# Optimization experiments

Measured on AMD Instinct MI355X. Metric: run time of the kernel, lower is better.

## Reference

```python
import jax, jax.numpy as jnp
import numpy as np


def _lstm(x, h0, c0, Wx, Wh, b):
    """Keras-order LSTM (gates i,f,c,o). x: [B,T,E] -> hidden seq [B,T,H]."""
    xw = jnp.einsum('bte,eg->btg', x, Wx) + b  # precompute input projections

    def step(carry, xw_t):
        h, c = carry
        z = xw_t + h @ Wh
        i, f, g, o = jnp.split(z, 4, axis=-1)
        c = jax.nn.sigmoid(f) * c + jax.nn.sigmoid(i) * jnp.tanh(g)
        h = jax.nn.sigmoid(o) * jnp.tanh(c)
        return (h, c), h

    _, hs = jax.lax.scan(step, (h0, c0), jnp.swapaxes(xw, 0, 1))
    return jnp.swapaxes(hs, 0, 1)


def setup_inputs() -> dict:
    key = jax.random.key(0)
    ks = jax.random.split(key, 16)
    V_IN = V_OUT = 32000
    E = 512      # embedding_dim
    H = 512      # encoder hidden_units per direction
    D = 2 * H    # decoder state width (matches BiLSTM output / attention dims)
    B, T_IN, T_OUT = 4, 128, 128
    s = 0.02

    def w(k, shape):
        return jax.random.normal(k, shape, jnp.float32) * s

    return {
        'input_seq': jax.random.randint(ks[0], (B, T_IN), 0, V_IN, jnp.int32),
        'output_seq': jax.random.randint(ks[1], (B, T_OUT), 0, V_OUT, jnp.int32),
        'enc_emb': w(ks[2], (V_IN, E)),
        'dec_emb': w(ks[3], (V_OUT, E)),
        'Wx_f': w(ks[4], (E, 4 * H)), 'Wh_f': w(ks[5], (H, 4 * H)), 'b_f': jnp.zeros((4 * H,), jnp.float32),
        'Wx_b': w(ks[6], (E, 4 * H)), 'Wh_b': w(ks[7], (H, 4 * H)), 'b_b': jnp.zeros((4 * H,), jnp.float32),
        'Wx_d': w(ks[8], (E, 4 * D)), 'Wh_d': w(ks[9], (D, 4 * D)), 'b_d': jnp.zeros((4 * D,), jnp.float32),
        'attn_scale': w(ks[10], (D,)),
        'Wo': w(ks[11], (D, V_OUT)), 'bo': jnp.zeros((V_OUT,), jnp.float32),
    }


def reference(input_seq, output_seq, enc_emb, dec_emb,
              Wx_f, Wh_f, b_f, Wx_b, Wh_b, b_b,
              Wx_d, Wh_d, b_d, attn_scale, Wo, bo):
    B = input_seq.shape[0]
    H = Wh_f.shape[0]
    D = 2 * H

    # --- encoder: BiLSTM, return_sequences=True ---
    enc_x = enc_emb[input_seq]                       # [B,Tin,E]
    z = jnp.zeros((B, H), jnp.float32)
    fwd = _lstm(enc_x, z, z, Wx_f, Wh_f, b_f)        # [B,Tin,H]
    bwd = _lstm(enc_x[:, ::-1], z, z, Wx_b, Wh_b, b_b)[:, ::-1]
    enc_out = jnp.concatenate([fwd, bwd], axis=-1)   # [B,Tin,2H]

    # --- decoder: LSTMCell-driven RNN, init state = last encoder output ---
    dec_x = dec_emb[output_seq]                      # [B,Tout,E]
    h0 = enc_out[:, -1, :]                           # [B,D]
    c0 = jnp.zeros((B, D), jnp.float32)
    dec_out = _lstm(dec_x, h0, c0, Wx_d, Wh_d, b_d)  # [B,Tout,D]

    # --- additive (Bahdanau) attention: query=dec_out, key=value=enc_out ---
    scores = jnp.einsum(
        'btsd,d->bts',
        jnp.tanh(dec_out[:, :, None, :] + enc_out[:, None, :, :]),
        attn_scale)                                  # [B,Tout,Tin]
    wts = jax.nn.softmax(scores, axis=-1)
    attn = jnp.einsum('bts,bsd->btd', wts, enc_out)  # [B,Tout,D]

    # --- output dense + softmax over vocab ---
    return jax.nn.softmax(attn @ Wo + bo, axis=-1)   # [B,Tout,V_out]
```

## Files before the change

### kernel.cpp

```cpp
#include <hip/hip_runtime.h>


typedef __attribute__((ext_vector_type(8))) short bf16x8;
typedef __attribute__((ext_vector_type(4))) float f32x4;

__device__ __forceinline__ short f2bf(float f) {
  unsigned u = __builtin_bit_cast(unsigned, f);
  u += 0x7fffu + ((u >> 16) & 1u);
  return (short)(u >> 16);
}
__device__ __forceinline__ float b2f(short s) {
  unsigned u = ((unsigned)(unsigned short)s) << 16;
  return __builtin_bit_cast(float, u);
}
__device__ __forceinline__ float sigf(float x) { return 1.f / (1.f + __expf(-x)); }
__device__ __forceinline__ float tanhf_fast(float x) {
  x = fminf(fmaxf(x, -15.f), 15.f);
  float e = __expf(2.f * x);
  return (e - 1.f) / (e + 1.f);
}

__device__ __forceinline__ unsigned ld_coh(const unsigned* p) {
  return __hip_atomic_load(p, __ATOMIC_RELAXED, __HIP_MEMORY_SCOPE_AGENT);
}
__device__ __forceinline__ void st_coh(unsigned* p, unsigned v) {
  __hip_atomic_store(p, v, __ATOMIC_RELAXED, __HIP_MEMORY_SCOPE_AGENT);
}

#define OFF_HBF   ((size_t)0)
#define OFF_HBB   (OFF_HBF + 2*2048*4)
#define OFF_HBD   (OFF_HBB + 2*2048*4)
#define OFF_ENCX  (OFF_HBD + 2*4096*4)
#define OFF_DECX  (OFF_ENCX + (size_t)64*512*8*2)
#define OFF_WXF   (OFF_DECX + (size_t)64*512*8*2)
#define OFF_WXB   (OFF_WXF + (size_t)512*2048*2)
#define OFF_WXD   (OFF_WXB + (size_t)512*2048*2)
#define OFF_WOS   (OFF_WXD + (size_t)512*4096*2)
#define OFF_XWF   (OFF_WOS + (size_t)1024*32000*2)
#define OFF_XWB   (OFF_XWF + (size_t)512*2048*4)
#define OFF_XWD   (OFF_XWB + (size_t)512*2048*4)
#define OFF_ENCO  (OFF_XWD + (size_t)512*4096*4)
#define OFF_ENCT  (OFF_ENCO + (size_t)4*128*1024*4)
#define OFF_DECO  (OFF_ENCT + (size_t)4*128*1024*4)
#define OFF_ATTN  (OFF_DECO + (size_t)4*128*1024*4)
#define OFF_LOG   (OFF_ATTN + (size_t)128*512*8*2)
#define WS_NEED   (OFF_LOG + (size_t)512*32000*2)

__device__ __forceinline__ void gather_body(const int* seq, const float* emb,
                                            short* dst, int bx, int by) {
  int m  = by * 64 + (threadIdx.x & 63);
  int e8 = bx * 4 + (threadIdx.x >> 6);
  int id = seq[m];
  const float* src = emb + (size_t)id * 512 + e8 * 8;
  bf16x8 v;
#pragma unroll
  for (int j = 0; j < 8; ++j) v[j] = f2bf(src[j]);
  *(bf16x8*)(dst + ((size_t)e8 * 512 + m) * 8) = v;
}

__device__ __forceinline__ void swz_body(const float* W, short* dst, int N,
                                         int k8, int n) {
  const float* src = W + (size_t)k8 * 8 * N + n;
  bf16x8 v;
#pragma unroll
  for (int j = 0; j < 8; ++j) v[j] = f2bf(src[(size_t)j * N]);
  *(bf16x8*)(dst + ((size_t)k8 * N + n) * 8) = v;
}

__device__ __forceinline__ void gemm_body(const short* __restrict__ A,
                                          const short* __restrict__ B,
                                          float* Cf, short* Cb,
                                          int M, int N, int K,
                                          int bx, int by, bool bf16out) {
  const int wv = threadIdx.x >> 6, lane = threadIdx.x & 63;
  const int q = lane >> 4, l15 = lane & 15;
  const int m0 = by * 128 + (wv >> 1) * 64;
  const int n0 = bx * 128 + (wv & 1) * 64;
  f32x4 acc[4][4];
#pragma unroll
  for (int i = 0; i < 4; ++i)
#pragma unroll
    for (int j = 0; j < 4; ++j) acc[i][j] = (f32x4){0.f, 0.f, 0.f, 0.f};
  const int KS = K >> 5;
  for (int ks = 0; ks < KS; ++ks) {
    const size_t k8 = (size_t)(ks * 4 + q);
    const short* Ap = A + (k8 * M + m0 + l15) * 8;
    const short* Bp = B + (k8 * N + n0 + l15) * 8;
    bf16x8 av[4], bv[4];
#pragma unroll
    for (int i = 0; i < 4; ++i) av[i] = *(const bf16x8*)(Ap + i * 128);
#pragma unroll
    for (int j = 0; j < 4; ++j) bv[j] = *(const bf16x8*)(Bp + j * 128);
#pragma unroll
    for (int i = 0; i < 4; ++i)
#pragma unroll
      for (int j = 0; j < 4; ++j)
        acc[i][j] = __builtin_amdgcn_mfma_f32_16x16x32_bf16(av[i], bv[j], acc[i][j], 0, 0, 0);
  }
#pragma unroll
  for (int i = 0; i < 4; ++i)
#pragma unroll
    for (int j = 0; j < 4; ++j)
#pragma unroll
      for (int r = 0; r < 4; ++r) {
        size_t idx = (size_t)(m0 + i * 16 + q * 4 + r) * N + (n0 + j * 16 + l15);
        if (bf16out) Cb[idx] = f2bf(acc[i][j][r]);
        else         Cf[idx] = acc[i][j][r];
      }
}

__global__ __launch_bounds__(256) void prep(
    const int* __restrict__ iseq, const int* __restrict__ oseq,
    const float* __restrict__ enc_emb, const float* __restrict__ dec_emb,
    const float* __restrict__ Wx_f, const float* __restrict__ Wx_b,
    const float* __restrict__ Wx_d,
    short* encx, short* decx, short* wxf_s, short* wxb_s, short* wxd_s) {
  int bid = blockIdx.x;
  if (bid < 128)        { gather_body(iseq, enc_emb, encx, bid & 15, bid >> 4); return; }
  if (bid < 256)        { int s = bid - 128;  gather_body(oseq, dec_emb, decx, s & 15, s >> 4); return; }
  if (bid < 768)        { int s = bid - 256;  swz_body(Wx_f, wxf_s, 2048, s >> 3, (s & 7) * 256 + threadIdx.x); return; }
  if (bid < 1280)       { int s = bid - 768;  swz_body(Wx_b, wxb_s, 2048, s >> 3, (s & 7) * 256 + threadIdx.x); return; }
  { int s = bid - 1280; swz_body(Wx_d, wxd_s, 4096, s >> 4, (s & 15) * 256 + threadIdx.x); }
}

__global__ __launch_bounds__(256) void xw_enc_gemm(
    const short* __restrict__ encx, const short* __restrict__ wxf_s,
    const short* __restrict__ wxb_s, float* xw_f, float* xw_b) {
  gemm_body(encx, blockIdx.z ? wxb_s : wxf_s, blockIdx.z ? xw_b : xw_f,
            nullptr, 512, 2048, 512, blockIdx.x, blockIdx.y, false);
}

__global__ __launch_bounds__(256, 1) void lstm_enc_fused(
    const float* __restrict__ Wh_f, const float* __restrict__ Wh_b,
    const float* __restrict__ xw_f, const float* __restrict__ xw_b,
    const float* __restrict__ b_f, const float* __restrict__ b_b,
    unsigned* hb_f, unsigned* hb_b, float* enc_out, float* encT,
    const short* __restrict__ decx, const short* __restrict__ wxd_s,
    float* xw_d, const float* __restrict__ Wo, short* wo_s) {
  const int bid = blockIdx.x;
  const int tid = threadIdx.x;
  if (bid >= 192) {
    int sb = bid - 192;
    int k8 = sb / 125, nb = sb - k8 * 125;
    swz_body(Wo, wo_s, 32000, k8, nb * 256 + tid);
    return;
  }
  if (bid >= 64) {
    int gb = bid - 64;
    gemm_body(decx, wxd_s, xw_d, nullptr, 512, 4096, 512, gb & 31, gb >> 5, false);
    return;
  }
  const int dir = bid >> 5;
  const int u0  = (bid & 31) * 16;
  const int w = tid >> 6, lane = tid & 63;
  const int q = lane >> 4, l15 = lane & 15;
  const float* Wh   = dir ? Wh_b : Wh_f;
  const float* xw   = dir ? xw_b : xw_f;
  const float* bias = dir ? b_b : b_f;
  unsigned* hb = dir ? hb_b : hb_f;

  __shared__ short hs[5][520];
  __shared__ float zb[4][4][16];
  __shared__ float cb[4][16];
  if (tid < 64) {
    cb[tid >> 4][tid & 15] = 0.f;
    st_coh(hb + (tid >> 4) * 512 + u0 + (tid & 15), 1u << 16);
  }
  for (int k = tid; k < 520; k += 256) hs[4][k] = 0;

  const int col = w * 512 + u0 + l15;
  const float bcol = bias[col];
  bf16x8 wfrag[16];
#pragma unroll
  for (int ks = 0; ks < 16; ++ks) {
    bf16x8 v;
#pragma unroll
    for (int jj = 0; jj < 8; ++jj) {
      int k = ks * 32 + q * 8 + jj;
      v[jj] = f2bf(Wh[(size_t)k * 2048 + col]);
    }
    wfrag[ks] = v;
  }
  const short* hp = hs[(l15 < 4) ? l15 : 4];
  float xwv[4];
  if (q == 0) {
    int tx0 = dir ? 127 : 0;
#pragma unroll
    for (int r = 0; r < 4; ++r) xwv[r] = xw[((size_t)(r * 128 + tx0)) * 2048 + col];
  }
  __syncthreads();

#pragma unroll 1
  for (int t = 0; t < 128; ++t) {
    const unsigned exp_ = (unsigned)(t + 1);
    const unsigned* src = hb + (t & 1) * 2048;
    unsigned v[8];
    bool ok;
    int guard = 0;
    do {
#pragma unroll
      for (int j = 0; j < 8; ++j) v[j] = ld_coh(src + j * 256 + tid);
      ok = true;
#pragma unroll
      for (int j = 0; j < 8; ++j) ok &= ((v[j] >> 16) == exp_);
      if (!ok) __builtin_amdgcn_s_sleep(1);
    } while (!ok && ++guard < (1 << 14));
#pragma unroll
    for (int j = 0; j < 8; ++j) {
      unsigned idx = j * 256 + tid;
      hs[idx >> 9][idx & 511] = (short)(v[j] & 0xffffu);
    }
    __syncthreads();

    f32x4 a0 = (f32x4){0.f, 0.f, 0.f, 0.f}, a1 = a0;
#pragma unroll
    for (int ks = 0; ks < 16; ks += 2) {
      bf16x8 f0 = *(const bf16x8*)(hp + ks * 32 + q * 8);
      bf16x8 f1 = *(const bf16x8*)(hp + (ks + 1) * 32 + q * 8);
      a0 = __builtin_amdgcn_mfma_f32_16x16x32_bf16(f0, wfrag[ks], a0, 0, 0, 0);
      a1 = __builtin_amdgcn_mfma_f32_16x16x32_bf16(f1, wfrag[ks + 1], a1, 0, 0, 0);
    }
    const int tx = dir ? (127 - t) : t;
    if (q == 0) {
#pragma unroll
      for (int r = 0; r < 4; ++r) zb[w][r][l15] = a0[r] + a1[r] + xwv[r] + bcol;
      if (t < 127) {
        int txn = dir ? (126 - t) : (t + 1);
#pragma unroll
        for (int r = 0; r < 4; ++r) xwv[r] = xw[((size_t)(r * 128 + txn)) * 2048 + col];
      }
    }
    __syncthreads();
    if (tid < 64) {
      int b = tid >> 4, u = tid & 15;
      float zi = zb[0][b][u], zf = zb[1][b][u], zg = zb[2][b][u], zo = zb[3][b][u];
      float c = sigf(zf) * cb[b][u] + sigf(zi) * tanhf_fast(zg);
      cb[b][u] = c;
      float h = sigf(zo) * tanhf_fast(c);
      if (t < 127)
        st_coh(hb + ((t + 1) & 1) * 2048 + b * 512 + u0 + u,
               ((unsigned)(t + 2) << 16) | (unsigned short)f2bf(h));
      int d = dir * 512 + u0 + u;
      enc_out[((size_t)(b * 128 + tx)) * 1024 + d] = h;
      encT[((size_t)(b * 1024 + d)) * 128 + tx] = h;
    }
  }
}

__global__ __launch_bounds__(256, 1) void lstm_dec(
    const float* __restrict__ Wh_d, const float* __restrict__ xw_d,
    const float* __restrict__ b_d, const float* __restrict__ enc_out,
    unsigned* hb, float* dec_out) {
  const int u0  = blockIdx.x * 16;
  const int tid = threadIdx.x;
  const int w = tid >> 6, lane = tid & 63;
  const int q = lane >> 4, l15 = lane & 15;

  __shared__ short hs[5][1032];
  __shared__ float zb[4][4][16];
  __shared__ float cb[4][16];
  if (tid < 64) {
    int b = tid >> 4, u = tid & 15;
    cb[b][u] = 0.f;
    float h0 = enc_out[((size_t)(b * 128 + 127)) * 1024 + u0 + u];
    st_coh(hb + b * 1024 + u0 + u, (1u << 16) | (unsigned short)f2bf(h0));
  }
  for (int k = tid; k < 1032; k += 256) hs[4][k] = 0;

  const int col = w * 1024 + u0 + l15;
  const float bcol = b_d[col];
  bf16x8 wfrag[32];
#pragma unroll
  for (int ks = 0; ks < 32; ++ks) {
    bf16x8 v;
#pragma unroll
    for (int jj = 0; jj < 8; ++jj) {
      int k = ks * 32 + q * 8 + jj;
      v[jj] = f2bf(Wh_d[(size_t)k * 4096 + col]);
    }
    wfrag[ks] = v;
  }
  const short* hp = hs[(l15 < 4) ? l15 : 4];
  float xwv[4];
  if (q == 0) {
#pragma unroll
    for (int r = 0; r < 4; ++r) xwv[r] = xw_d[((size_t)(r * 128)) * 4096 + col];
  }
  __syncthreads();

#pragma unroll 1
  for (int t = 0; t < 128; ++t) {
    const unsigned exp_ = (unsigned)(t + 1);
    const unsigned* src = hb + (t & 1) * 4096;
    unsigned v[16];
    bool ok;
    int guard = 0;
    do {
#pragma unroll
      for (int j = 0; j < 16; ++j) v[j] = ld_coh(src + j * 256 + tid);
      ok = true;
#pragma unroll
      for (int j = 0; j < 16; ++j) ok &= ((v[j] >> 16) == exp_);
      if (!ok) __builtin_amdgcn_s_sleep(1);
    } while (!ok && ++guard < (1 << 14));
#pragma unroll
    for (int j = 0; j < 16; ++j) {
      unsigned idx = j * 256 + tid;
      hs[idx >> 10][idx & 1023] = (short)(v[j] & 0xffffu);
    }
    __syncthreads();

    f32x4 a0 = (f32x4){0.f, 0.f, 0.f, 0.f}, a1 = a0;
#pragma unroll
    for (int ks = 0; ks < 32; ks += 2) {
      bf16x8 f0 = *(const bf16x8*)(hp + ks * 32 + q * 8);
      bf16x8 f1 = *(const bf16x8*)(hp + (ks + 1) * 32 + q * 8);
      a0 = __builtin_amdgcn_mfma_f32_16x16x32_bf16(f0, wfrag[ks], a0, 0, 0, 0);
      a1 = __builtin_amdgcn_mfma_f32_16x16x32_bf16(f1, wfrag[ks + 1], a1, 0, 0, 0);
    }
    if (q == 0) {
#pragma unroll
      for (int r = 0; r < 4; ++r) zb[w][r][l15] = a0[r] + a1[r] + xwv[r] + bcol;
      if (t < 127) {
#pragma unroll
        for (int r = 0; r < 4; ++r) xwv[r] = xw_d[((size_t)(r * 128 + t + 1)) * 4096 + col];
      }
    }
    __syncthreads();
    if (tid < 64) {
      int b = tid >> 4, u = tid & 15;
      float zi = zb[0][b][u], zf = zb[1][b][u], zg = zb[2][b][u], zo = zb[3][b][u];
      float c = sigf(zf) * cb[b][u] + sigf(zi) * tanhf_fast(zg);
      cb[b][u] = c;
      float h = sigf(zo) * tanhf_fast(c);
      if (t < 127)
        st_coh(hb + ((t + 1) & 1) * 4096 + b * 1024 + u0 + u,
               ((unsigned)(t + 2) << 16) | (unsigned short)f2bf(h));
      dec_out[((size_t)(b * 128 + t)) * 1024 + u0 + u] = h;
    }
  }
}

__global__ __launch_bounds__(256) void attention(
    const float* __restrict__ dec_out, const float* __restrict__ enc_out,
    const float* __restrict__ encT, const float* __restrict__ scale,
    short* __restrict__ attn_swz) {
  const int m = blockIdx.x, b = m >> 7, tid = threadIdx.x;
  __shared__ float dec_s[1024], scl_s[1024];
  __shared__ float red[256], wts[128], sred[2];
  for (int d = tid; d < 1024; d += 256) {
    dec_s[d] = dec_out[(size_t)m * 1024 + d];
    scl_s[d] = scale[d];
  }
  __syncthreads();
  const int s = tid & 127, half = tid >> 7;
  float sc = 0.f;
  const float* ep = encT + (size_t)b * 1024 * 128 + s;
  for (int d = half * 512; d < half * 512 + 512; ++d)
    sc += tanhf_fast(dec_s[d] + ep[(size_t)d * 128]) * scl_s[d];
  red[tid] = sc;
  __syncthreads();
  float v = 0.f;
  if (tid < 128) { v = red[tid] + red[tid + 128]; wts[tid] = v; }
  __syncthreads();
  if (tid < 64) {
    float mx = fmaxf(wts[tid], wts[tid + 64]);
    for (int off = 32; off; off >>= 1) mx = fmaxf(mx, __shfl_down(mx, off));
    if (tid == 0) sred[0] = mx;
  }
  __syncthreads();
  const float MX = sred[0];
  if (tid < 128) { v = __expf(v - MX); wts[tid] = v; }
  __syncthreads();
  if (tid < 64) {
    float sm = wts[tid] + wts[tid + 64];
    for (int off = 32; off; off >>= 1) sm += __shfl_down(sm, off);
    if (tid == 0) sred[1] = sm;
  }
  __syncthreads();
  const float inv = 1.f / sred[1];
  if (tid < 128) wts[tid] = v * inv;
  __syncthreads();
#pragma unroll
  for (int kk = 0; kk < 4; ++kk) {
    int d = tid + kk * 256;
    float a = 0.f;
    for (int ss = 0; ss < 128; ++ss)
      a += wts[ss] * enc_out[((size_t)(b * 128 + ss)) * 1024 + d];
    attn_swz[((size_t)(d >> 3) * 512 + m) * 8 + (d & 7)] = f2bf(a);
  }
}

__global__ __launch_bounds__(256) void gemm_wo(const short* __restrict__ attn_s,
                                               const short* __restrict__ wo_s,
                                               short* logits) {
  gemm_body(attn_s, wo_s, nullptr, logits, 512, 32000, 1024,
            blockIdx.x, blockIdx.y, true);
}

__global__ __launch_bounds__(256) void softmax_out(const short* __restrict__ logits,
                                                   const float* __restrict__ bo,
                                                   float* __restrict__ out) {
  const int m = blockIdx.x, tid = threadIdx.x;
  __shared__ float red[256];
  const short* lp = logits + (size_t)m * 32000;
  float mx = -1e30f;
  for (int n = tid; n < 32000; n += 256) mx = fmaxf(mx, b2f(lp[n]) + bo[n]);
  red[tid] = mx;
  __syncthreads();
  for (int s2 = 128; s2 > 0; s2 >>= 1) {
    if (tid < s2) red[tid] = fmaxf(red[tid], red[tid + s2]);
    __syncthreads();
  }
  const float M = red[0];
  __syncthreads();
  float sm = 0.f;
  for (int n = tid; n < 32000; n += 256) sm += __expf(b2f(lp[n]) + bo[n] - M);
  red[tid] = sm;
  __syncthreads();
  for (int s2 = 128; s2 > 0; s2 >>= 1) {
    if (tid < s2) red[tid] += red[tid + s2];
    __syncthreads();
  }
  const float inv = 1.f / red[0];
  for (int n = tid; n < 32000; n += 256)
    out[(size_t)m * 32000 + n] = __expf(b2f(lp[n]) + bo[n] - M) * inv;
}

extern "C" void kernel_launch(void* const* d_in, const int* in_sizes, int n_in,
                              void* d_out, int out_size, void* d_ws, size_t ws_size,
                              hipStream_t stream) {
  (void)in_sizes; (void)n_in; (void)out_size;
  if (ws_size < WS_NEED) return;

  const int*   input_seq  = (const int*)d_in[0];
  const int*   output_seq = (const int*)d_in[1];
  const float* enc_emb    = (const float*)d_in[2];
  const float* dec_emb    = (const float*)d_in[3];
  const float* Wx_f = (const float*)d_in[4];
  const float* Wh_f = (const float*)d_in[5];
  const float* b_f  = (const float*)d_in[6];
  const float* Wx_b = (const float*)d_in[7];
  const float* Wh_b = (const float*)d_in[8];
  const float* b_b  = (const float*)d_in[9];
  const float* Wx_d = (const float*)d_in[10];
  const float* Wh_d = (const float*)d_in[11];
  const float* b_d  = (const float*)d_in[12];
  const float* attn_scale = (const float*)d_in[13];
  const float* Wo   = (const float*)d_in[14];
  const float* bo   = (const float*)d_in[15];
  float* out = (float*)d_out;

  char* ws = (char*)d_ws;
  unsigned* hbf   = (unsigned*)(ws + OFF_HBF);
  unsigned* hbb   = (unsigned*)(ws + OFF_HBB);
  unsigned* hbd   = (unsigned*)(ws + OFF_HBD);
  short* encx     = (short*)(ws + OFF_ENCX);
  short* decx     = (short*)(ws + OFF_DECX);
  short* wxf_s    = (short*)(ws + OFF_WXF);
  short* wxb_s    = (short*)(ws + OFF_WXB);
  short* wxd_s    = (short*)(ws + OFF_WXD);
  short* wo_s     = (short*)(ws + OFF_WOS);
  float* xw_f     = (float*)(ws + OFF_XWF);
  float* xw_b     = (float*)(ws + OFF_XWB);
  float* xw_d     = (float*)(ws + OFF_XWD);
  float* enc_out  = (float*)(ws + OFF_ENCO);
  float* encT     = (float*)(ws + OFF_ENCT);
  float* dec_out  = (float*)(ws + OFF_DECO);
  short* attn_s   = (short*)(ws + OFF_ATTN);
  short* logits   = (short*)(ws + OFF_LOG);


  prep<<<2304, 256, 0, stream>>>(input_seq, output_seq, enc_emb, dec_emb,
                                 Wx_f, Wx_b, Wx_d, encx, decx, wxf_s, wxb_s, wxd_s);
  xw_enc_gemm<<<dim3(16, 4, 2), 256, 0, stream>>>(encx, wxf_s, wxb_s, xw_f, xw_b);
  lstm_enc_fused<<<64 + 128 + 16000, 256, 0, stream>>>(
      Wh_f, Wh_b, xw_f, xw_b, b_f, b_b, hbf, hbb, enc_out, encT,
      decx, wxd_s, xw_d, Wo, wo_s);
  lstm_dec<<<64, 256, 0, stream>>>(Wh_d, xw_d, b_d, enc_out, hbd, dec_out);
  attention<<<512, 256, 0, stream>>>(dec_out, enc_out, encT, attn_scale, attn_s);
  gemm_wo<<<dim3(250, 4), 256, 0, stream>>>(attn_s, wo_s, logits);
  softmax_out<<<512, 256, 0, stream>>>(logits, bo, out);
}
```

Before: 1.173 ms.

## Fuse encoder and decoder LSTMs into one persistent kernel with register-level gate math

Moves the decoder input-projection GEMM into a single combined xw GEMM launch. It then runs encoder and decoder LSTM blocks in the same kernel, with the decoder blocks spinning until the encoder publishes the final hidden state through the coherent buffer. Each lane's column now maps to an interleaved (gate, unit) layout, so activations are computed in all lanes and combined via wave shuffles instead of a shared-memory round trip and a 64-thread tail. This removes one kernel launch boundary and per-step LDS staging and serialization. It risks deadlock if decoder blocks occupy CUs before the encoder blocks get scheduled, and it adds extra spin latency.

```diff
diff --git a/kernel.cpp b/kernel.cpp
--- a/kernel.cpp
+++ b/kernel.cpp
@@ -123,52 +123,41 @@
   { int s = bid - 1280; swz_body(Wx_d, wxd_s, 4096, s >> 4, (s & 15) * 256 + threadIdx.x); }
 }
 
-__global__ __launch_bounds__(256) void xw_enc_gemm(
+__global__ __launch_bounds__(256) void xw_all_gemm(
     const short* __restrict__ encx, const short* __restrict__ wxf_s,
-    const short* __restrict__ wxb_s, float* xw_f, float* xw_b) {
-  gemm_body(encx, blockIdx.z ? wxb_s : wxf_s, blockIdx.z ? xw_b : xw_f,
-            nullptr, 512, 2048, 512, blockIdx.x, blockIdx.y, false);
-}
-
-__global__ __launch_bounds__(256, 1) void lstm_enc_fused(
+    const short* __restrict__ wxb_s, float* xw_f, float* xw_b,
+    const short* __restrict__ decx, const short* __restrict__ wxd_s,
+    float* xw_d) {
+  int bid = blockIdx.x;
+  if (bid < 64)       { gemm_body(encx, wxf_s, xw_f, nullptr, 512, 2048, 512, bid & 15, bid >> 4, false); return; }
+  if (bid < 128)      { int s = bid - 64;  gemm_body(encx, wxb_s, xw_b, nullptr, 512, 2048, 512, s & 15, s >> 4, false); return; }
+  { int g = bid - 128; gemm_body(decx, wxd_s, xw_d, nullptr, 512, 4096, 512, g & 31, g >> 5, false); }
+}
+
+__device__ __forceinline__ void lstm_enc_block(
     const float* __restrict__ Wh_f, const float* __restrict__ Wh_b,
     const float* __restrict__ xw_f, const float* __restrict__ xw_b,
     const float* __restrict__ b_f, const float* __restrict__ b_b,
-    unsigned* hb_f, unsigned* hb_b, float* enc_out, float* encT,
-    const short* __restrict__ decx, const short* __restrict__ wxd_s,
-    float* xw_d, const float* __restrict__ Wo, short* wo_s) {
-  const int bid = blockIdx.x;
+    unsigned* hb_f, unsigned* hb_b, unsigned* hbd,
+    float* enc_out, float* encT, int slice) {
+  const int dir = slice >> 5;
+  const int u0  = (slice & 31) * 16;
   const int tid = threadIdx.x;
-  if (bid >= 192) {
-    int sb = bid - 192;
-    int k8 = sb / 125, nb = sb - k8 * 125;
-    swz_body(Wo, wo_s, 32000, k8, nb * 256 + tid);
-    return;
-  }
-  if (bid >= 64) {
-    int gb = bid - 64;
-    gemm_body(decx, wxd_s, xw_d, nullptr, 512, 4096, 512, gb & 31, gb >> 5, false);
-    return;
-  }
-  const int dir = bid >> 5;
-  const int u0  = (bid & 31) * 16;
   const int w = tid >> 6, lane = tid & 63;
   const int q = lane >> 4, l15 = lane & 15;
+  const int gate = l15 & 3, du = l15 >> 2;
+  const int unit = u0 + w * 4 + du;
   const float* Wh   = dir ? Wh_b : Wh_f;
   const float* xw   = dir ? xw_b : xw_f;
   const float* bias = dir ? b_b : b_f;
   unsigned* hb = dir ? hb_b : hb_f;
 
-  __shared__ short hs[5][520];
-  __shared__ float zb[4][4][16];
-  __shared__ float cb[4][16];
-  if (tid < 64) {
-    cb[tid >> 4][tid & 15] = 0.f;
-    st_coh(hb + (tid >> 4) * 512 + u0 + (tid & 15), 1u << 16);
-  }
+  __shared__ __align__(16) short hs[5][520];
+  if (q == 0)
+    st_coh(hb + gate * 512 + unit, 1u << 16);
   for (int k = tid; k < 520; k += 256) hs[4][k] = 0;
 
-  const int col = w * 512 + u0 + l15;
+  const int col = gate * 512 + unit;
   const float bcol = bias[col];
   bf16x8 wfrag[16];
 #pragma unroll
@@ -183,11 +172,12 @@
   }
   const short* hp = hs[(l15 < 4) ? l15 : 4];
   float xwv[4];
-  if (q == 0) {
+  {
     int tx0 = dir ? 127 : 0;
 #pragma unroll
     for (int r = 0; r < 4; ++r) xwv[r] = xw[((size_t)(r * 128 + tx0)) * 2048 + col];
   }
+  float c[4] = {0.f, 0.f, 0.f, 0.f};
   __syncthreads();
 
 #pragma unroll 1
@@ -221,53 +211,61 @@
       a1 = __builtin_amdgcn_mfma_f32_16x16x32_bf16(f1, wfrag[ks + 1], a1, 0, 0, 0);
     }
     const int tx = dir ? (127 - t) : t;
+    float y[4];
+#pragma unroll
+    for (int r = 0; r < 4; ++r) {
+      float z = a0[r] + a1[r] + xwv[r] + bcol;
+      y[r] = (gate == 2) ? tanhf_fast(z) : sigf(z);
+    }
+    if (t < 127) {
+      int txn = dir ? (126 - t) : (t + 1);
+#pragma unroll
+      for (int r = 0; r < 4; ++r) xwv[r] = xw[((size_t)(r * 128 + txn)) * 2048 + col];
+    }
+    const int gb = lane & ~3;
+    float yi[4], yf[4], yg[4], yo[4];
+#pragma unroll
+    for (int r = 0; r < 4; ++r) {
+      yi[r] = __shfl(y[r], gb);
+      yf[r] = __shfl(y[r], gb + 1);
+      yg[r] = __shfl(y[r], gb + 2);
+      yo[r] = __shfl(y[r], gb + 3);
+    }
+#pragma unroll
+    for (int r = 0; r < 4; ++r) c[r] = yf[r] * c[r] + yi[r] * yg[r];
+    float cg = c[0], yog = yo[0];
+    cg  = (gate == 1) ? c[1]  : cg;  cg  = (gate == 2) ? c[2]  : cg;  cg  = (gate == 3) ? c[3]  : cg;
+    yog = (gate == 1) ? yo[1] : yog; yog = (gate == 2) ? yo[2] : yog; yog = (gate == 3) ? yo[3] : yog;
+    const float hv = yog * tanhf_fast(cg);
     if (q == 0) {
-#pragma unroll
-      for (int r = 0; r < 4; ++r) zb[w][r][l15] = a0[r] + a1[r] + xwv[r] + bcol;
-      if (t < 127) {
-        int txn = dir ? (126 - t) : (t + 1);
-#pragma unroll
-        for (int r = 0; r < 4; ++r) xwv[r] = xw[((size_t)(r * 128 + txn)) * 2048 + col];
-      }
+      const int b = gate, d = dir * 512 + unit;
+      const unsigned short hb16 = (unsigned short)f2bf(hv);
+      if (t < 127)
+        st_coh(hb + ((t + 1) & 1) * 2048 + b * 512 + unit,
+               ((unsigned)(t + 2) << 16) | hb16);
+      if ((dir == 0 && t == 127) || (dir == 1 && t == 0))
+        st_coh(hbd + b * 1024 + d, (1u << 16) | hb16);
+      enc_out[((size_t)(b * 128 + tx)) * 1024 + d] = hv;
+      encT[((size_t)(b * 1024 + d)) * 128 + tx] = hv;
     }
     __syncthreads();
-    if (tid < 64) {
-      int b = tid >> 4, u = tid & 15;
-      float zi = zb[0][b][u], zf = zb[1][b][u], zg = zb[2][b][u], zo = zb[3][b][u];
-      float c = sigf(zf) * cb[b][u] + sigf(zi) * tanhf_fast(zg);
-      cb[b][u] = c;
-      float h = sigf(zo) * tanhf_fast(c);
-      if (t < 127)
-        st_coh(hb + ((t + 1) & 1) * 2048 + b * 512 + u0 + u,
-               ((unsigned)(t + 2) << 16) | (unsigned short)f2bf(h));
-      int d = dir * 512 + u0 + u;
-      enc_out[((size_t)(b * 128 + tx)) * 1024 + d] = h;
-      encT[((size_t)(b * 1024 + d)) * 128 + tx] = h;
-    }
-  }
-}
-
-__global__ __launch_bounds__(256, 1) void lstm_dec(
+  }
+}
+
+__device__ __forceinline__ void lstm_dec_block(
     const float* __restrict__ Wh_d, const float* __restrict__ xw_d,
-    const float* __restrict__ b_d, const float* __restrict__ enc_out,
-    unsigned* hb, float* dec_out) {
-  const int u0  = blockIdx.x * 16;
+    const float* __restrict__ b_d, unsigned* hb, float* dec_out, int slice) {
+  const int u0  = slice * 16;
   const int tid = threadIdx.x;
   const int w = tid >> 6, lane = tid & 63;
   const int q = lane >> 4, l15 = lane & 15;
-
-  __shared__ short hs[5][1032];
-  __shared__ float zb[4][4][16];
-  __shared__ float cb[4][16];
-  if (tid < 64) {
-    int b = tid >> 4, u = tid & 15;
-    cb[b][u] = 0.f;
-    float h0 = enc_out[((size_t)(b * 128 + 127)) * 1024 + u0 + u];
-    st_coh(hb + b * 1024 + u0 + u, (1u << 16) | (unsigned short)f2bf(h0));
-  }
+  const int gate = l15 & 3, du = l15 >> 2;
+  const int unit = u0 + w * 4 + du;
+
+  __shared__ __align__(16) short hs[5][1032];
   for (int k = tid; k < 1032; k += 256) hs[4][k] = 0;
 
-  const int col = w * 1024 + u0 + l15;
+  const int col = gate * 1024 + unit;
   const float bcol = b_d[col];
   bf16x8 wfrag[32];
 #pragma unroll
@@ -282,9 +280,13 @@
   }
   const short* hp = hs[(l15 < 4) ? l15 : 4];
   float xwv[4];
-  if (q == 0) {
-#pragma unroll
-    for (int r = 0; r < 4; ++r) xwv[r] = xw_d[((size_t)(r * 128)) * 4096 + col];
+#pragma unroll
+  for (int r = 0; r < 4; ++r) xwv[r] = xw_d[((size_t)(r * 128)) * 4096 + col];
+  float c[4] = {0.f, 0.f, 0.f, 0.f};
+
+  if (tid == 0) {
+    int g = 0;
+    while ((ld_coh(hb) >> 16) != 1u && ++g < (1 << 14)) __builtin_amdgcn_s_sleep(64);
   }
   __syncthreads();
 
@@ -318,27 +320,63 @@
       a0 = __builtin_amdgcn_mfma_f32_16x16x32_bf16(f0, wfrag[ks], a0, 0, 0, 0);
       a1 = __builtin_amdgcn_mfma_f32_16x16x32_bf16(f1, wfrag[ks + 1], a1, 0, 0, 0);
     }
+    float y[4];
+#pragma unroll
+    for (int r = 0; r < 4; ++r) {
+      float z = a0[r] + a1[r] + xwv[r] + bcol;
+      y[r] = (gate == 2) ? tanhf_fast(z) : sigf(z);
+    }
+    if (t < 127) {
+#pragma unroll
+      for (int r = 0; r < 4; ++r) xwv[r] = xw_d[((size_t)(r * 128 + t + 1)) * 4096 + col];
+    }
+    const int gb = lane & ~3;
+    float yi[4], yf[4], yg[4], yo[4];
+#pragma unroll
+    for (int r = 0; r < 4; ++r) {
+      yi[r] = __shfl(y[r], gb);
+      yf[r] = __shfl(y[r], gb + 1);
+      yg[r] = __shfl(y[r], gb + 2);
+      yo[r] = __shfl(y[r], gb + 3);
+    }
+#pragma unroll
+    for (int r = 0; r < 4; ++r) c[r] = yf[r] * c[r] + yi[r] * yg[r];
+    float cg = c[0], yog = yo[0];
+    cg  = (gate == 1) ? c[1]  : cg;  cg  = (gate == 2) ? c[2]  : cg;  cg  = (gate == 3) ? c[3]  : cg;
+    yog = (gate == 1) ? yo[1] : yog; yog = (gate == 2) ? yo[2] : yog; yog = (gate == 3) ? yo[3] : yog;
+    const float hv = yog * tanhf_fast(cg);
     if (q == 0) {
-#pragma unroll
-      for (int r = 0; r < 4; ++r) zb[w][r][l15] = a0[r] + a1[r] + xwv[r] + bcol;
-      if (t < 127) {
-#pragma unroll
-        for (int r = 0; r < 4; ++r) xwv[r] = xw_d[((size_t)(r * 128 + t + 1)) * 4096 + col];
-      }
+      const int b = gate;
+      if (t < 127)
+        st_coh(hb + ((t + 1) & 1) * 4096 + b * 1024 + unit,
+               ((unsigned)(t + 2) << 16) | (unsigned short)f2bf(hv));
+      dec_out[((size_t)(b * 128 + t)) * 1024 + unit] = hv;
     }
     __syncthreads();
-    if (tid < 64) {
-      int b = tid >> 4, u = tid & 15;
-      float zi = zb[0][b][u], zf = zb[1][b][u], zg = zb[2][b][u], zo = zb[3][b][u];
-      float c = sigf(zf) * cb[b][u] + sigf(zi) * tanhf_fast(zg);
-      cb[b][u] = c;
-      float h = sigf(zo) * tanhf_fast(c);
-      if (t < 127)
-        st_coh(hb + ((t + 1) & 1) * 4096 + b * 1024 + u0 + u,
-               ((unsigned)(t + 2) << 16) | (unsigned short)f2bf(h));
-      dec_out[((size_t)(b * 128 + t)) * 1024 + u0 + u] = h;
-    }
-  }
+  }
+}
+
+__global__ __launch_bounds__(256, 1) void lstm_fused(
+    const float* __restrict__ Wh_f, const float* __restrict__ Wh_b,
+    const float* __restrict__ xw_f, const float* __restrict__ xw_b,
+    const float* __restrict__ b_f, const float* __restrict__ b_b,
+    unsigned* hb_f, unsigned* hb_b, unsigned* hbd, float* enc_out, float* encT,
+    const float* __restrict__ Wh_d, const float* __restrict__ xw_d,
+    const float* __restrict__ b_d, float* dec_out,
+    const float* __restrict__ Wo, short* wo_s) {
+  const int bid = blockIdx.x;
+  if (bid >= 128) {
+    int sb = bid - 128;
+    int k8 = sb / 125, nb = sb - k8 * 125;
+    swz_body(Wo, wo_s, 32000, k8, nb * 256 + threadIdx.x);
+    return;
+  }
+  if (bid >= 64) {
+    lstm_dec_block(Wh_d, xw_d, b_d, hbd, dec_out, bid - 64);
+    return;
+  }
+  lstm_enc_block(Wh_f, Wh_b, xw_f, xw_b, b_f, b_b, hb_f, hb_b, hbd,
+                 enc_out, encT, bid);
 }
 
 __global__ __launch_bounds__(256) void attention(
@@ -473,11 +511,11 @@
 
   prep<<<2304, 256, 0, stream>>>(input_seq, output_seq, enc_emb, dec_emb,
                                  Wx_f, Wx_b, Wx_d, encx, decx, wxf_s, wxb_s, wxd_s);
-  xw_enc_gemm<<<dim3(16, 4, 2), 256, 0, stream>>>(encx, wxf_s, wxb_s, xw_f, xw_b);
-  lstm_enc_fused<<<64 + 128 + 16000, 256, 0, stream>>>(
-      Wh_f, Wh_b, xw_f, xw_b, b_f, b_b, hbf, hbb, enc_out, encT,
-      decx, wxd_s, xw_d, Wo, wo_s);
-  lstm_dec<<<64, 256, 0, stream>>>(Wh_d, xw_d, b_d, enc_out, hbd, dec_out);
+  xw_all_gemm<<<256, 256, 0, stream>>>(encx, wxf_s, wxb_s, xw_f, xw_b,
+                                       decx, wxd_s, xw_d);
+  lstm_fused<<<128 + 16000, 256, 0, stream>>>(
+      Wh_f, Wh_b, xw_f, xw_b, b_f, b_b, hbf, hbb, hbd, enc_out, encT,
+      Wh_d, xw_d, b_d, dec_out, Wo, wo_s);
   attention<<<512, 256, 0, stream>>>(dec_out, enc_out, encT, attn_scale, attn_s);
   gemm_wo<<<dim3(250, 4), 256, 0, stream>>>(attn_s, wo_s, logits);
   softmax_out<<<512, 256, 0, stream>>>(logits, bo, out);
```

Result: slower. 1.255 ms (+7.0%).
